# Performance work log

Measured on AMD Instinct MI355X. Metric: run time of the kernel, lower is better.

The kernel has to match this reference:

```python
import jax, jax.numpy as jnp
import numpy as np

B, N, D = 4096, 32768, 256


def setup_inputs() -> dict:
    key = jax.random.key(0)
    kx, kp = jax.random.split(key)
    x = jax.random.normal(kx, (B, D), dtype=jnp.float32)
    prototypes = jax.random.normal(kp, (N, D), dtype=jnp.float32)
    return {"x": x, "prototypes": prototypes}


def reference(x, prototypes):
    # Brute-force L2 1-NN: faiss IndexFlatL2 exact search, k=1, then gather
    x_sq = jnp.sum(x * x, axis=-1, keepdims=True)            # [B, 1]
    p_sq = jnp.sum(prototypes * prototypes, axis=-1)          # [N]
    dists = x_sq + p_sq[None, :] - 2.0 * (x @ prototypes.T)   # [B, N]
    idx = jnp.argmin(dists, axis=-1)                          # [B]
    return prototypes[idx]                                    # [B, D]
```

## Files before the change

kernel.cpp:

```cpp
#include <hip/hip_runtime.h>
#include <stdint.h>


#define NB 4096
#define NP 32768
#define ND 256
#define NG 512
#define MARGIN 2.0f
#define NSPLIT 8
#define CPB 4096

typedef __attribute__((ext_vector_type(8))) __bf16 bf16x8;
typedef __attribute__((ext_vector_type(4))) __bf16 bf16x4;
typedef __attribute__((ext_vector_type(4))) float f32x4;

static constexpr size_t OFF_PSQ = 0;
static constexpr size_t OFF_XB  = 131072;
static constexpr size_t OFF_PB  = OFF_XB + (size_t)NB * ND * 2;
static constexpr size_t OFF_BM  = OFF_PB + (size_t)NP * ND * 2;
static constexpr size_t WS_NEED = OFF_BM + (size_t)NB * NG * 4;

#define VMCNT(n) asm volatile("s_waitcnt vmcnt(" #n ")" ::: "memory")
#define LGKM0()  asm volatile("s_waitcnt lgkmcnt(0)" ::: "memory")

__device__ __forceinline__ void gload_lds16(const void* g, void* l) {
    __builtin_amdgcn_global_load_lds(
        (const __attribute__((address_space(1))) uint32_t*)g,
        (__attribute__((address_space(3))) uint32_t*)l, 16, 0, 0);
}
__device__ __forceinline__ unsigned fkey(float f) {
    unsigned u = __float_as_uint(f);
    return (u & 0x80000000u) ? ~u : (u | 0x80000000u);
}
__device__ __forceinline__ float fkey_inv(unsigned u) {
    unsigned o = (u & 0x80000000u) ? (u & 0x7FFFFFFFu) : ~u;
    return __uint_as_float(o);
}
__device__ __forceinline__ unsigned long long umin64(unsigned long long a,
                                                     unsigned long long b) {
    return a < b ? a : b;
}
__device__ __forceinline__ unsigned umin32(unsigned a, unsigned b) {
    return a < b ? a : b;
}

__global__ void prep_kernel(const float* __restrict__ X, const float* __restrict__ P,
                            float* __restrict__ psq, __bf16* __restrict__ Xb,
                            __bf16* __restrict__ Pb) {
    int row  = blockIdx.x * 4 + (threadIdx.x >> 6);
    int lane = threadIdx.x & 63;
    if (row < NP) {
        f32x4 v = ((const f32x4*)(P + (size_t)row * ND))[lane];
        bf16x4 b;
        b.x = (__bf16)v.x; b.y = (__bf16)v.y; b.z = (__bf16)v.z; b.w = (__bf16)v.w;
        ((bf16x4*)(Pb + (size_t)row * ND))[lane] = b;
        float s = v.x*v.x + v.y*v.y + v.z*v.z + v.w*v.w;
        #pragma unroll
        for (int off = 32; off > 0; off >>= 1) s += __shfl_down(s, off);
        if (lane == 0) psq[row] = s;
    } else {
        int r = row - NP;
        f32x4 v = ((const f32x4*)(X + (size_t)r * ND))[lane];
        bf16x4 b;
        b.x = (__bf16)v.x; b.y = (__bf16)v.y; b.z = (__bf16)v.z; b.w = (__bf16)v.w;
        ((bf16x4*)(Xb + (size_t)r * ND))[lane] = b;
    }
}

__global__ __launch_bounds__(512, 2)
void nn_alds_kernel(const __bf16* __restrict__ Xb, const __bf16* __restrict__ Pb,
                    const float* __restrict__ psq,
                    unsigned* __restrict__ blockmin) {
    __shared__ __align__(16) char smem[147456];
    char*  ring    = smem;
    char*  A_lds   = smem + 65536;
    float* psq_lds = (float*)(smem + 131072);

    const int tid  = threadIdx.x;
    const int lane = tid & 63;
    const int wave = tid >> 6;
    const int wm = wave >> 2, wn = wave & 3;
    const int bid    = blockIdx.x;
    const int nsplit = bid & 7;
    const int mblk   = bid >> 3;
    const int bm     = mblk * 128;
    const int Nb     = nsplit * CPB;
    const int fr = lane & 15, kg = lane >> 4;
    const int wbase16 = (tid & ~63) * 16;

    f32x4 acc[4][4];
    #pragma unroll
    for (int i = 0; i < 4; ++i)
        #pragma unroll
        for (int j = 0; j < 4; ++j) acc[i][j] = (f32x4){0.f, 0.f, 0.f, 0.f};

    auto stage = [&](int p) {
        char* dst = ring + (size_t)(p & 3) * 16384;
        const int colb = Nb + (p >> 3) * 256;
        const int kq   = p & 7;
        #pragma unroll
        for (int i = 0; i < 2; ++i) {
            const int c = i * 512 + tid;
            const int fn = c >> 6;
            const int l  = c & 63;
            gload_lds16(Pb + (size_t)(colb + fn * 16 + (l & 15)) * ND +
                            kq * 32 + (l >> 4) * 8,
                        dst + i * 8192 + wbase16);
        }
    };

    #pragma unroll
    for (int i = 0; i < 8; ++i) {
        const int c  = i * 512 + tid;
        const int q  = c >> 9;
        const int fm = (c >> 6) & 7;
        const int l  = c & 63;
        gload_lds16(Xb + (size_t)(bm + fm * 16 + (l & 15)) * ND +
                        q * 32 + (l >> 4) * 8,
                    A_lds + (size_t)(i * 512) * 16 + wbase16);
    }
    gload_lds16((const char*)(psq + Nb) + (size_t)tid * 16,
                (char*)psq_lds + wbase16);
    gload_lds16((const char*)(psq + Nb) + 8192 + (size_t)tid * 16,
                (char*)psq_lds + 8192 + wbase16);
    stage(0); stage(1); stage(2);
    VMCNT(4);
    __builtin_amdgcn_s_barrier();
    __builtin_amdgcn_sched_barrier(0);

    bf16x8 av[2][4], bv[2][4];
    #pragma unroll
    for (int mi = 0; mi < 4; ++mi)
        av[0][mi] = *(const bf16x8*)(A_lds +
            (size_t)(((0 * 8) + (wm * 4 + mi)) * 64 + lane) * 16);
    #pragma unroll
    for (int ni = 0; ni < 4; ++ni)
        bv[0][ni] = *(const bf16x8*)(ring +
            (size_t)((wn * 4 + ni) * 64 + lane) * 16);

    auto epi = [&](int nt) {
        float cq[4];
        #pragma unroll
        for (int ni = 0; ni < 4; ++ni)
            cq[ni] = psq_lds[nt * 256 + wn * 64 + ni * 16 + fr];
        const int g = nsplit * 64 + nt * 4 + wn;
        #pragma unroll
        for (int mi = 0; mi < 4; ++mi) {
            #pragma unroll
            for (int r = 0; r < 4; ++r) {
                float d = fmaf(-2.f, acc[mi][0][r], cq[0]);
                #pragma unroll
                for (int ni = 1; ni < 4; ++ni)
                    d = fminf(d, fmaf(-2.f, acc[mi][ni][r], cq[ni]));
                #pragma unroll
                for (int m = 1; m < 16; m <<= 1)
                    d = fminf(d, __shfl_xor(d, m));
                if (fr == 0)
                    blockmin[(size_t)(bm + wm * 64 + mi * 16 + kg * 4 + r) * NG
                             + g] = fkey(d);
            }
        }
        #pragma unroll
        for (int i = 0; i < 4; ++i)
            #pragma unroll
            for (int j = 0; j < 4; ++j)
                acc[i][j] = (f32x4){0.f, 0.f, 0.f, 0.f};
    };

    #pragma unroll 1
    for (int nt = 0; nt < 15; ++nt) {
        #pragma unroll
        for (int q = 0; q < 8; ++q) {
            const int cur = q & 1, nxt = cur ^ 1;
            const int t = nt * 8 + q;
            const int qn = (q + 1) & 7;
            VMCNT(2);
            __builtin_amdgcn_s_barrier();
            __builtin_amdgcn_sched_barrier(0);
            const char* pc = ring + (size_t)((t + 1) & 3) * 16384;
            #pragma unroll
            for (int ni = 0; ni < 4; ++ni)
                bv[nxt][ni] = *(const bf16x8*)(pc +
                    (size_t)((wn * 4 + ni) * 64 + lane) * 16);
            #pragma unroll
            for (int mi = 0; mi < 4; ++mi)
                av[nxt][mi] = *(const bf16x8*)(A_lds +
                    (size_t)((qn * 8 + wm * 4 + mi) * 64 + lane) * 16);
            stage(t + 3);
            __builtin_amdgcn_s_setprio(1);
            #pragma unroll
            for (int mi = 0; mi < 4; ++mi)
                #pragma unroll
                for (int ni = 0; ni < 4; ++ni)
                    acc[mi][ni] = __builtin_amdgcn_mfma_f32_16x16x32_bf16(
                        av[cur][mi], bv[cur][ni], acc[mi][ni], 0, 0, 0);
            __builtin_amdgcn_s_setprio(0);
            if (q == 7) epi(nt);
        }
    }
    #pragma unroll
    for (int q = 0; q < 8; ++q) {
        const int cur = q & 1, nxt = cur ^ 1;
        const int t = 120 + q;
        const int qn = (q + 1) & 7;
        if (q <= 5) { VMCNT(2); }
        else        { VMCNT(0); }
        __builtin_amdgcn_s_barrier();
        __builtin_amdgcn_sched_barrier(0);
        if (q < 7) {
            const char* pc = ring + (size_t)((t + 1) & 3) * 16384;
            #pragma unroll
            for (int ni = 0; ni < 4; ++ni)
                bv[nxt][ni] = *(const bf16x8*)(pc +
                    (size_t)((wn * 4 + ni) * 64 + lane) * 16);
            #pragma unroll
            for (int mi = 0; mi < 4; ++mi)
                av[nxt][mi] = *(const bf16x8*)(A_lds +
                    (size_t)((qn * 8 + wm * 4 + mi) * 64 + lane) * 16);
            if (q <= 4) stage(t + 3);
        }
        __builtin_amdgcn_s_setprio(1);
        #pragma unroll
        for (int mi = 0; mi < 4; ++mi)
            #pragma unroll
            for (int ni = 0; ni < 4; ++ni)
                acc[mi][ni] = __builtin_amdgcn_mfma_f32_16x16x32_bf16(
                    av[cur][mi], bv[cur][ni], acc[mi][ni], 0, 0, 0);
        __builtin_amdgcn_s_setprio(0);
        if (q == 7) epi(15);
    }
}

__global__ __launch_bounds__(512, 2)
void rescore_wave_kernel(const float* __restrict__ X, const float* __restrict__ P,
                         const float* __restrict__ psq,
                         const unsigned* __restrict__ blockmin,
                         float* __restrict__ out) {
    __shared__ float Xs[8][256];
    __shared__ unsigned short wcand[8][512];
    __shared__ int wcnt[8];

    const int tid = threadIdx.x, lane = tid & 63, wv = tid >> 6;
    const int row = blockIdx.x * 8 + wv;

    ((f32x4*)Xs[wv])[lane] = ((const f32x4*)(X + (size_t)row * ND))[lane];
    if (lane == 0) wcnt[wv] = 0;

    const unsigned* bmr = blockmin + (size_t)row * NG;
    uint4 ka = ((const uint4*)bmr)[lane * 2];
    uint4 kb = ((const uint4*)bmr)[lane * 2 + 1];
    unsigned km = umin32(umin32(umin32(ka.x, ka.y), umin32(ka.z, ka.w)),
                         umin32(umin32(kb.x, kb.y), umin32(kb.z, kb.w)));
    #pragma unroll
    for (int m = 1; m < 64; m <<= 1) km = umin32(km, __shfl_xor(km, m));
    const unsigned thr = fkey(fkey_inv(km) + MARGIN);

    const unsigned k8[8] = {ka.x, ka.y, ka.z, ka.w, kb.x, kb.y, kb.z, kb.w};
    #pragma unroll
    for (int i = 0; i < 8; ++i)
        if (k8[i] <= thr)
            wcand[wv][atomicAdd(&wcnt[wv], 1)] = (unsigned short)(lane * 8 + i);
    LGKM0();
    const int n = wcnt[wv];

    unsigned long long best = 0xFFFFFFFFFFFFFFFFull;
    const f32x4* x4 = (const f32x4*)Xs[wv];
    for (int c = 0; c < n; ++c) {
        const int col = (int)wcand[wv][c] * 64 + lane;
        const f32x4* p4 = (const f32x4*)(P + (size_t)col * ND);
        float s = 0.f;
        #pragma unroll 16
        for (int i = 0; i < 64; ++i) {
            f32x4 pv = p4[i], xv = x4[i];
            s = fmaf(xv.x, pv.x, s); s = fmaf(xv.y, pv.y, s);
            s = fmaf(xv.z, pv.z, s); s = fmaf(xv.w, pv.w, s);
        }
        float d = fmaf(-2.f, s, psq[col]);
        best = umin64(best, ((unsigned long long)fkey(d) << 32) |
                            (unsigned long long)(unsigned)col);
    }
    #pragma unroll
    for (int m = 1; m < 64; m <<= 1)
        best = umin64(best, __shfl_xor(best, m));
    const unsigned bc = (unsigned)(best & 0xFFFFFFFFull);
    ((f32x4*)(out + (size_t)row * ND))[lane] =
        ((const f32x4*)(P + (size_t)bc * ND))[lane];
}

#define BM1 128
#define BN1 128
#define BK1 32
#define LDA1 132

__global__ void psq_init_kernel(const float* __restrict__ P, float* __restrict__ psq,
                                unsigned long long* __restrict__ minpack) {
    int row  = blockIdx.x * 4 + (threadIdx.x >> 6);
    int lane = threadIdx.x & 63;
    float4 p4 = ((const float4*)(P + (size_t)row * ND))[lane];
    float s = p4.x*p4.x + p4.y*p4.y + p4.z*p4.z + p4.w*p4.w;
    #pragma unroll
    for (int off = 32; off > 0; off >>= 1) s += __shfl_down(s, off);
    if (lane == 0) psq[row] = s;
    int gid = blockIdx.x * blockDim.x + threadIdx.x;
    if (gid < NB) minpack[gid] = 0xFFFFFFFFFFFFFFFFull;
}

__global__ __launch_bounds__(256, 2)
void nn_main_kernel(const float* __restrict__ X, const float* __restrict__ P,
                    const float* __restrict__ psq,
                    unsigned long long* __restrict__ minpack) {
    __shared__ __align__(16) char smem_raw[2 * BK1 * LDA1 * 4];
    float (*As)[LDA1] = (float (*)[LDA1])smem_raw;
    float (*Bs)[LDA1] = (float (*)[LDA1])(smem_raw + BK1 * LDA1 * 4);
    const int bm  = blockIdx.y * BM1;
    const int bn  = blockIdx.x * BN1;
    const int tid = threadIdx.x;
    const int tx  = tid & 15;
    const int ty  = tid >> 4;
    float acc[8][8];
    #pragma unroll
    for (int i = 0; i < 8; ++i)
        #pragma unroll
        for (int j = 0; j < 8; ++j) acc[i][j] = 0.f;
    const int lrow = tid >> 3;
    const int lk   = (tid & 7) * 4;
    for (int k0 = 0; k0 < ND; k0 += BK1) {
        #pragma unroll
        for (int p = 0; p < 4; ++p) {
            int r = p * 32 + lrow;
            float4 aa = *(const float4*)(X + (size_t)(bm + r) * ND + k0 + lk);
            As[lk+0][r] = aa.x; As[lk+1][r] = aa.y; As[lk+2][r] = aa.z; As[lk+3][r] = aa.w;
            float4 bb = *(const float4*)(P + (size_t)(bn + r) * ND + k0 + lk);
            Bs[lk+0][r] = bb.x; Bs[lk+1][r] = bb.y; Bs[lk+2][r] = bb.z; Bs[lk+3][r] = bb.w;
        }
        __syncthreads();
        #pragma unroll 4
        for (int k = 0; k < BK1; ++k) {
            float4 a0 = *(const float4*)&As[k][ty*8];
            float4 a1 = *(const float4*)&As[k][ty*8 + 4];
            float4 b0 = *(const float4*)&Bs[k][tx*4];
            float4 b1 = *(const float4*)&Bs[k][64 + tx*4];
            float av2[8] = {a0.x,a0.y,a0.z,a0.w,a1.x,a1.y,a1.z,a1.w};
            float bv2[8] = {b0.x,b0.y,b0.z,b0.w,b1.x,b1.y,b1.z,b1.w};
            #pragma unroll
            for (int i = 0; i < 8; ++i)
                #pragma unroll
                for (int j = 0; j < 8; ++j)
                    acc[i][j] = fmaf(av2[i], bv2[j], acc[i][j]);
        }
        __syncthreads();
    }
    unsigned long long (*red)[16] = (unsigned long long (*)[16])smem_raw;
    float cj[8];
    int   jglob[8];
    #pragma unroll
    for (int j = 0; j < 8; ++j) {
        int c = (j < 4) ? (tx*4 + j) : (64 + tx*4 + (j - 4));
        jglob[j] = bn + c;
        cj[j]    = psq[bn + c];
    }
    #pragma unroll
    for (int i = 0; i < 8; ++i) {
        float bestv = 0.f; unsigned bidx = 0u; bool first = true;
        #pragma unroll
        for (int j = 0; j < 8; ++j) {
            float s = fmaf(-2.f, acc[i][j], cj[j]);
            if (first || s < bestv) { bestv = s; bidx = (unsigned)jglob[j]; first = false; }
        }
        unsigned u = fkey(bestv);
        red[ty*8 + i][tx] = ((unsigned long long)u << 32) | (unsigned long long)bidx;
    }
    __syncthreads();
    if (tid < BM1) {
        unsigned long long m = red[tid][0];
        #pragma unroll
        for (int t = 1; t < 16; ++t) m = umin64(m, red[tid][t]);
        atomicMin(&minpack[bm + tid], m);
    }
}

__global__ void gather_kernel(const float* __restrict__ P,
                              const unsigned long long* __restrict__ minpack,
                              float* __restrict__ out) {
    int row = blockIdx.x;
    unsigned idx = (unsigned)(minpack[row] & 0xFFFFFFFFull);
    int lane = threadIdx.x;
    ((float4*)(out + (size_t)row * ND))[lane] =
        ((const float4*)(P + (size_t)idx * ND))[lane];
}

extern "C" void kernel_launch(void* const* d_in, const int* in_sizes, int n_in,
                              void* d_out, int out_size, void* d_ws, size_t ws_size,
                              hipStream_t stream) {
    const float* X = (const float*)d_in[0];
    const float* P = (const float*)d_in[1];
    float* out = (float*)d_out;
    char* w = (char*)d_ws;

    if (ws_size >= WS_NEED) {
        float* psq = (float*)(w + OFF_PSQ);
        __bf16* Xb = (__bf16*)(w + OFF_XB);
        __bf16* Pb = (__bf16*)(w + OFF_PB);
        unsigned* blockmin = (unsigned*)(w + OFF_BM);

        prep_kernel<<<(NP + NB) / 4, 256, 0, stream>>>(X, P, psq, Xb, Pb);
        nn_alds_kernel<<<(NB / 128) * NSPLIT, 512, 0, stream>>>(Xb, Pb, psq,
                                                                blockmin);
        rescore_wave_kernel<<<NB / 8, 512, 0, stream>>>(X, P, psq, blockmin, out);
    } else {
        float* psq = (float*)w;
        unsigned long long* minpack = (unsigned long long*)(w + (size_t)NP * 4);
        psq_init_kernel<<<NP / 4, 256, 0, stream>>>(P, psq, minpack);
        dim3 grid(NP / BN1, NB / BM1);
        nn_main_kernel<<<grid, dim3(256), 0, stream>>>(X, P, psq, minpack);
        gather_kernel<<<NB, 64, 0, stream>>>(P, minpack, out);
    }
}
```

Baseline: 184.9 us.

## Shrink M tile, keep X fragments in registers, raise occupancy

```diff
diff --git a/kernel.cpp b/kernel.cpp
--- a/kernel.cpp
+++ b/kernel.cpp
@@ -67,14 +67,11 @@
     }
 }
 
-__global__ __launch_bounds__(512, 2)
-void nn_alds_kernel(const __bf16* __restrict__ Xb, const __bf16* __restrict__ Pb,
-                    const float* __restrict__ psq,
-                    unsigned* __restrict__ blockmin) {
-    __shared__ __align__(16) char smem[147456];
-    char*  ring    = smem;
-    char*  A_lds   = smem + 65536;
-    float* psq_lds = (float*)(smem + 131072);
+__global__ __launch_bounds__(512, 4)
+void nn_tlp_kernel(const __bf16* __restrict__ Xb, const __bf16* __restrict__ Pb,
+                   const float* __restrict__ psq,
+                   unsigned* __restrict__ blockmin) {
+    __shared__ __align__(16) char ring[65536];
 
     const int tid  = threadIdx.x;
     const int lane = tid & 63;
@@ -83,14 +80,22 @@
     const int bid    = blockIdx.x;
     const int nsplit = bid & 7;
     const int mblk   = bid >> 3;
-    const int bm     = mblk * 128;
+    const int bm     = mblk * 64;
     const int Nb     = nsplit * CPB;
     const int fr = lane & 15, kg = lane >> 4;
     const int wbase16 = (tid & ~63) * 16;
 
-    f32x4 acc[4][4];
-    #pragma unroll
-    for (int i = 0; i < 4; ++i)
+    bf16x8 a[2][8];
+    #pragma unroll
+    for (int mi = 0; mi < 2; ++mi)
+        #pragma unroll
+        for (int q = 0; q < 8; ++q)
+            a[mi][q] = *(const bf16x8*)(Xb +
+                (size_t)(bm + wm * 32 + mi * 16 + fr) * ND + q * 32 + kg * 8);
+
+    f32x4 acc[2][4];
+    #pragma unroll
+    for (int i = 0; i < 2; ++i)
         #pragma unroll
         for (int j = 0; j < 4; ++j) acc[i][j] = (f32x4){0.f, 0.f, 0.f, 0.f};
 
@@ -109,125 +114,64 @@
         }
     };
 
-    #pragma unroll
-    for (int i = 0; i < 8; ++i) {
-        const int c  = i * 512 + tid;
-        const int q  = c >> 9;
-        const int fm = (c >> 6) & 7;
-        const int l  = c & 63;
-        gload_lds16(Xb + (size_t)(bm + fm * 16 + (l & 15)) * ND +
-                        q * 32 + (l >> 4) * 8,
-                    A_lds + (size_t)(i * 512) * 16 + wbase16);
-    }
-    gload_lds16((const char*)(psq + Nb) + (size_t)tid * 16,
-                (char*)psq_lds + wbase16);
-    gload_lds16((const char*)(psq + Nb) + 8192 + (size_t)tid * 16,
-                (char*)psq_lds + 8192 + wbase16);
     stage(0); stage(1); stage(2);
-    VMCNT(4);
-    __builtin_amdgcn_s_barrier();
-    __builtin_amdgcn_sched_barrier(0);
-
-    bf16x8 av[2][4], bv[2][4];
-    #pragma unroll
-    for (int mi = 0; mi < 4; ++mi)
-        av[0][mi] = *(const bf16x8*)(A_lds +
-            (size_t)(((0 * 8) + (wm * 4 + mi)) * 64 + lane) * 16);
-    #pragma unroll
-    for (int ni = 0; ni < 4; ++ni)
-        bv[0][ni] = *(const bf16x8*)(ring +
-            (size_t)((wn * 4 + ni) * 64 + lane) * 16);
-
-    auto epi = [&](int nt) {
-        float cq[4];
-        #pragma unroll
-        for (int ni = 0; ni < 4; ++ni)
-            cq[ni] = psq_lds[nt * 256 + wn * 64 + ni * 16 + fr];
-        const int g = nsplit * 64 + nt * 4 + wn;
-        #pragma unroll
-        for (int mi = 0; mi < 4; ++mi) {
-            #pragma unroll
-            for (int r = 0; r < 4; ++r) {
-                float d = fmaf(-2.f, acc[mi][0][r], cq[0]);
-                #pragma unroll
-                for (int ni = 1; ni < 4; ++ni)
-                    d = fminf(d, fmaf(-2.f, acc[mi][ni][r], cq[ni]));
-                #pragma unroll
-                for (int m = 1; m < 16; m <<= 1)
-                    d = fminf(d, __shfl_xor(d, m));
-                if (fr == 0)
-                    blockmin[(size_t)(bm + wm * 64 + mi * 16 + kg * 4 + r) * NG
-                             + g] = fkey(d);
-            }
-        }
-        #pragma unroll
-        for (int i = 0; i < 4; ++i)
-            #pragma unroll
-            for (int j = 0; j < 4; ++j)
-                acc[i][j] = (f32x4){0.f, 0.f, 0.f, 0.f};
-    };
 
     #pragma unroll 1
-    for (int nt = 0; nt < 15; ++nt) {
+    for (int nt = 0; nt < 16; ++nt) {
         #pragma unroll
         for (int q = 0; q < 8; ++q) {
-            const int cur = q & 1, nxt = cur ^ 1;
             const int t = nt * 8 + q;
-            const int qn = (q + 1) & 7;
-            VMCNT(2);
+            if (t < 126)       { VMCNT(4); }
+            else if (t == 126) { VMCNT(2); }
+            else               { VMCNT(0); }
             __builtin_amdgcn_s_barrier();
             __builtin_amdgcn_sched_barrier(0);
-            const char* pc = ring + (size_t)((t + 1) & 3) * 16384;
+            if (t <= 124) stage(t + 3);
+            const char* pc = ring + (size_t)(t & 3) * 16384;
+            bf16x8 bv[4];
             #pragma unroll
             for (int ni = 0; ni < 4; ++ni)
-                bv[nxt][ni] = *(const bf16x8*)(pc +
+                bv[ni] = *(const bf16x8*)(pc +
                     (size_t)((wn * 4 + ni) * 64 + lane) * 16);
-            #pragma unroll
-            for (int mi = 0; mi < 4; ++mi)
-                av[nxt][mi] = *(const bf16x8*)(A_lds +
-                    (size_t)((qn * 8 + wm * 4 + mi) * 64 + lane) * 16);
-            stage(t + 3);
             __builtin_amdgcn_s_setprio(1);
             #pragma unroll
-            for (int mi = 0; mi < 4; ++mi)
+            for (int mi = 0; mi < 2; ++mi)
                 #pragma unroll
                 for (int ni = 0; ni < 4; ++ni)
                     acc[mi][ni] = __builtin_amdgcn_mfma_f32_16x16x32_bf16(
-                        av[cur][mi], bv[cur][ni], acc[mi][ni], 0, 0, 0);
+                        a[mi][q], bv[ni], acc[mi][ni], 0, 0, 0);
             __builtin_amdgcn_s_setprio(0);
-            if (q == 7) epi(nt);
-        }
-    }
-    #pragma unroll
-    for (int q = 0; q < 8; ++q) {
-        const int cur = q & 1, nxt = cur ^ 1;
-        const int t = 120 + q;
-        const int qn = (q + 1) & 7;
-        if (q <= 5) { VMCNT(2); }
-        else        { VMCNT(0); }
-        __builtin_amdgcn_s_barrier();
-        __builtin_amdgcn_sched_barrier(0);
-        if (q < 7) {
-            const char* pc = ring + (size_t)((t + 1) & 3) * 16384;
-            #pragma unroll
-            for (int ni = 0; ni < 4; ++ni)
-                bv[nxt][ni] = *(const bf16x8*)(pc +
-                    (size_t)((wn * 4 + ni) * 64 + lane) * 16);
-            #pragma unroll
-            for (int mi = 0; mi < 4; ++mi)
-                av[nxt][mi] = *(const bf16x8*)(A_lds +
-                    (size_t)((qn * 8 + wm * 4 + mi) * 64 + lane) * 16);
-            if (q <= 4) stage(t + 3);
-        }
-        __builtin_amdgcn_s_setprio(1);
-        #pragma unroll
-        for (int mi = 0; mi < 4; ++mi)
-            #pragma unroll
-            for (int ni = 0; ni < 4; ++ni)
-                acc[mi][ni] = __builtin_amdgcn_mfma_f32_16x16x32_bf16(
-                    av[cur][mi], bv[cur][ni], acc[mi][ni], 0, 0, 0);
-        __builtin_amdgcn_s_setprio(0);
-        if (q == 7) epi(15);
+
+            if (q == 7) {
+                const int colb = Nb + nt * 256 + wn * 64;
+                float cq[4];
+                #pragma unroll
+                for (int ni = 0; ni < 4; ++ni)
+                    cq[ni] = psq[colb + ni * 16 + fr];
+                const int g = nsplit * 64 + nt * 4 + wn;
+                #pragma unroll
+                for (int mi = 0; mi < 2; ++mi) {
+                    #pragma unroll
+                    for (int r = 0; r < 4; ++r) {
+                        float d = fmaf(-2.f, acc[mi][0][r], cq[0]);
+                        #pragma unroll
+                        for (int ni = 1; ni < 4; ++ni)
+                            d = fminf(d, fmaf(-2.f, acc[mi][ni][r], cq[ni]));
+                        #pragma unroll
+                        for (int m = 1; m < 16; m <<= 1)
+                            d = fminf(d, __shfl_xor(d, m));
+                        if (fr == 0)
+                            blockmin[(size_t)(bm + wm * 32 + mi * 16 + kg * 4
+                                              + r) * NG + g] = fkey(d);
+                    }
+                }
+                #pragma unroll
+                for (int i = 0; i < 2; ++i)
+                    #pragma unroll
+                    for (int j = 0; j < 4; ++j)
+                        acc[i][j] = (f32x4){0.f, 0.f, 0.f, 0.f};
+            }
+        }
     }
 }
 
@@ -404,8 +348,8 @@
         unsigned* blockmin = (unsigned*)(w + OFF_BM);
 
         prep_kernel<<<(NP + NB) / 4, 256, 0, stream>>>(X, P, psq, Xb, Pb);
-        nn_alds_kernel<<<(NB / 128) * NSPLIT, 512, 0, stream>>>(Xb, Pb, psq,
-                                                                blockmin);
+        nn_tlp_kernel<<<(NB / 64) * NSPLIT, 512, 0, stream>>>(Xb, Pb, psq,
+                                                              blockmin);
         rescore_wave_kernel<<<NB / 8, 512, 0, stream>>>(X, P, psq, blockmin, out);
     } else {
         float* psq = (float*)w;
```

Measured after the change: 271.4 us. 46.8% more time.
